# Kernel optimization log

Hardware: AMD Instinct MI355X
Metric: run time of the kernel (lower is better)

The kernel has to match this reference:

```python
import jax, jax.numpy as jnp
import numpy as np


def _conv_valid(x, w):
    # x: [B, Cin, H, W], w: [Cout, Cin, K, K], stride 1, no padding
    return jax.lax.conv_general_dilated(
        x, w, window_strides=(1, 1), padding='VALID',
        dimension_numbers=('NCHW', 'OIHW', 'NCHW'))


def _buggy_maxpool(x, k=2):
    # Faithful to the source MaxPool: window of size kxk slides with STRIDE 1,
    # but only the first H//k x W//k positions are kept (top-left region).
    nh = x.shape[2] // k
    nw = x.shape[3] // k
    m = jax.lax.reduce_window(
        x, -jnp.inf, jax.lax.max,
        window_dimensions=(1, 1, k, k),
        window_strides=(1, 1, 1, 1),
        padding='VALID')  # [B, C, H-k+1, W-k+1]
    return m[:, :, :nh, :nw]


def setup_inputs() -> dict:
    key = jax.random.key(0)
    ks = jax.random.split(key, 9)
    B = 8192
    x = jax.random.normal(ks[0], (B, 3, 32, 32), dtype=jnp.float32)
    s = 0.1
    conv1_w = jax.random.normal(ks[1], (6, 3, 5, 5), dtype=jnp.float32) * s
    conv2_w = jax.random.normal(ks[2], (16, 6, 5, 5), dtype=jnp.float32) * s
    fc1_w = jax.random.normal(ks[3], (120, 400), dtype=jnp.float32) * s
    fc1_b = jax.random.normal(ks[4], (120,), dtype=jnp.float32) * s
    fc2_w = jax.random.normal(ks[5], (84, 120), dtype=jnp.float32) * s
    fc2_b = jax.random.normal(ks[6], (84,), dtype=jnp.float32) * s
    fc3_w = jax.random.normal(ks[7], (10, 84), dtype=jnp.float32) * s
    fc3_b = jax.random.normal(ks[8], (10,), dtype=jnp.float32) * s
    return {
        'x': x,
        'conv1_w': conv1_w, 'conv2_w': conv2_w,
        'fc1_w': fc1_w, 'fc1_b': fc1_b,
        'fc2_w': fc2_w, 'fc2_b': fc2_b,
        'fc3_w': fc3_w, 'fc3_b': fc3_b,
    }


def reference(x, conv1_w, conv2_w, fc1_w, fc1_b, fc2_w, fc2_b, fc3_w, fc3_b):
    h = _buggy_maxpool(jax.nn.relu(_conv_valid(x, conv1_w)))   # [B,6,14,14]
    h = _buggy_maxpool(jax.nn.relu(_conv_valid(h, conv2_w)))   # [B,16,5,5]
    h = h.reshape(-1, 16 * 5 * 5)                              # [B,400]
    h = jax.nn.relu(h @ fc1_w.T + fc1_b)                       # [B,120]
    h = jax.nn.relu(h @ fc2_w.T + fc2_b)                       # [B,84]
    return h @ fc3_w.T + fc3_b                                 # [B,10]
```

## Files before the change

kernel.cpp:

```cpp
#include <hip/hip_runtime.h>


typedef float v2f __attribute__((ext_vector_type(2)));
__device__ __forceinline__ v2f mk2(float a, float b) { v2f t; t.x = a; t.y = b; return t; }
__device__ __forceinline__ v2f shfl2(v2f v, int src) {
    v2f r; r.x = __shfl(v.x, src, 64); r.y = __shfl(v.y, src, 64); return r;
}

constexpr int THREADS = 256;
constexpr int IPB = 4;

constexpr int W1P_OFF = 0;
constexpr int W2P_OFF = 452;
constexpr int IMG_BASE = 2852;
constexpr int XS_OFF = 0;
constexpr int P1_OFF = 0;
constexpr int P2_OFF = 900;
constexpr int F1_OFF = 0;
constexpr int F2_OFF = 128;
constexpr int IMG_STRIDE = 1300;
constexpr int LDS_FLOATS = IMG_BASE + IPB * IMG_STRIDE;

__device__ __forceinline__ void wave_sync() {
    asm volatile("s_waitcnt lgkmcnt(0)" ::: "memory");
}

extern "C" __global__ __launch_bounds__(THREADS, 4)
void lenet_fused(const float* __restrict__ x,
                 const float* __restrict__ w1,
                 const float* __restrict__ w2,
                 const float* __restrict__ fc1w, const float* __restrict__ fc1b,
                 const float* __restrict__ fc2w, const float* __restrict__ fc2b,
                 const float* __restrict__ fc3w, const float* __restrict__ fc3b,
                 float* __restrict__ out)
{
    __shared__ __align__(16) float lds[LDS_FLOATS];
    const int tid  = threadIdx.x;
    const int lane = tid & 63;
    const int wv   = tid >> 6;
    const int img0 = blockIdx.x * IPB;
    const v2f zero2 = mk2(0.f, 0.f);

    for (int i = tid; i < 450; i += THREADS) {
        int ocp = i / 150, rem = i - ocp * 150, k = rem >> 1, h = rem & 1;
        lds[W1P_OFF + i] = w1[(2 * ocp + h) * 75 + k];
    }
    for (int i = tid; i < 2400; i += THREADS) {
        int ocp = i / 300, rem = i - ocp * 300, k = rem >> 1, h = rem & 1;
        lds[W2P_OFF + i] = w2[(2 * ocp + h) * 150 + k];
    }

    float* base = lds + IMG_BASE + wv * IMG_STRIDE;
    {
        const float4* xg = (const float4*)(x + (size_t)(img0 + wv) * 3072);
        float4* xs4 = (float4*)(base + XS_OFF);
        for (int i = lane; i < 225; i += 64) {
            int c = i / 75, rem = i - c * 75;
            int r = rem / 5, c4 = rem - r * 5;
            xs4[i] = xg[c * 256 + r * 8 + c4];
        }
    }
    __syncthreads();

    float* p1 = base + P1_OFF;

    {
        const int l   = (lane < 33) ? lane : 32;
        const int ocp = l / 11;
        const int r   = l - ocp * 11;
        const float4* xs4 = (const float4*)(base + XS_OFF);
        const v2f* w1p = (const v2f*)(lds + W1P_OFF);

        v2f acc[11];
        #pragma unroll
        for (int c = 0; c < 11; ++c) acc[c] = zero2;

        float4 Xa = xs4[r * 5 + 0], Xb = xs4[r * 5 + 1],
               Xc = xs4[r * 5 + 2], Xd = xs4[r * 5 + 3];
        v2f W0[5];
        #pragma unroll
        for (int kc = 0; kc < 5; ++kc) W0[kc] = w1p[ocp * 75 + kc];

        #pragma unroll
        for (int i = 0; i < 15; ++i) {
            float4 Na, Nb, Nc, Nd; v2f W1r[5];
            if (i < 14) {
                const int ci = (i + 1) / 5, kr = (i + 1) % 5;
                const int b = ci * 75 + (r + kr) * 5;
                Na = xs4[b]; Nb = xs4[b + 1]; Nc = xs4[b + 2]; Nd = xs4[b + 3];
                #pragma unroll
                for (int kc = 0; kc < 5; ++kc)
                    W1r[kc] = w1p[ocp * 75 + (i + 1) * 5 + kc];
            }
            float xv[16];
            xv[0]=Xa.x; xv[1]=Xa.y; xv[2]=Xa.z;  xv[3]=Xa.w;
            xv[4]=Xb.x; xv[5]=Xb.y; xv[6]=Xb.z;  xv[7]=Xb.w;
            xv[8]=Xc.x; xv[9]=Xc.y; xv[10]=Xc.z; xv[11]=Xc.w;
            xv[12]=Xd.x; xv[13]=Xd.y; xv[14]=Xd.z; xv[15]=Xd.w;
            #pragma unroll
            for (int kc = 0; kc < 5; ++kc)
                #pragma unroll
                for (int c = 0; c < 11; ++c)
                    acc[c] = __builtin_elementwise_fma(
                        mk2(xv[c + kc], xv[c + kc]), W0[kc], acc[c]);
            if (i < 14) {
                Xa = Na; Xb = Nb; Xc = Nc; Xd = Nd;
                #pragma unroll
                for (int kc = 0; kc < 5; ++kc) W0[kc] = W1r[kc];
            }
        }

        v2f a[11], pm[10], m[10];
        #pragma unroll
        for (int c = 0; c < 11; ++c) a[c] = __builtin_elementwise_max(acc[c], zero2);
        #pragma unroll
        for (int c = 0; c < 10; ++c) pm[c] = __builtin_elementwise_max(a[c], a[c + 1]);
        #pragma unroll
        for (int c = 0; c < 10; ++c)
            m[c] = __builtin_elementwise_max(pm[c], shfl2(pm[c], lane + 1));
        wave_sync();
        if (r < 10) {
            const int oc0 = ocp * 2;
            float2* d0 = (float2*)(p1 + oc0 * 120 + r * 12);
            float2* d1 = (float2*)(p1 + (oc0 + 1) * 120 + r * 12);
            #pragma unroll
            for (int j = 0; j < 5; ++j) {
                d0[j] = make_float2(m[2 * j].x, m[2 * j + 1].x);
                d1[j] = make_float2(m[2 * j].y, m[2 * j + 1].y);
            }
        }
    }
    wave_sync();

    float* p2 = base + P2_OFF;
    {
        const int l   = (lane < 48) ? lane : 47;
        const int ocp = l / 6;
        const int r   = l - ocp * 6;
        const float4* p14 = (const float4*)p1;
        const float2* p12 = (const float2*)p1;
        const v2f* w2p = (const v2f*)(lds + W2P_OFF);

        v2f acc[6];
        #pragma unroll
        for (int c = 0; c < 6; ++c) acc[c] = zero2;

        float4 Xa = p14[r * 3 + 0], Xb = p14[r * 3 + 1];
        float2 Xc = p12[r * 6 + 4];
        v2f W0[5];
        #pragma unroll
        for (int kc = 0; kc < 5; ++kc) W0[kc] = w2p[ocp * 150 + kc];

        #pragma unroll
        for (int i = 0; i < 30; ++i) {
            float4 Na, Nb; float2 Nc; v2f W1r[5];
            if (i < 29) {
                const int ci = (i + 1) / 5, kr = (i + 1) % 5;
                Na = p14[ci * 30 + (r + kr) * 3 + 0];
                Nb = p14[ci * 30 + (r + kr) * 3 + 1];
                Nc = p12[ci * 60 + (r + kr) * 6 + 4];
                #pragma unroll
                for (int kc = 0; kc < 5; ++kc)
                    W1r[kc] = w2p[ocp * 150 + (i + 1) * 5 + kc];
            }
            float xv[10];
            xv[0]=Xa.x; xv[1]=Xa.y; xv[2]=Xa.z; xv[3]=Xa.w;
            xv[4]=Xb.x; xv[5]=Xb.y; xv[6]=Xb.z; xv[7]=Xb.w;
            xv[8]=Xc.x; xv[9]=Xc.y;
            #pragma unroll
            for (int kc = 0; kc < 5; ++kc)
                #pragma unroll
                for (int c = 0; c < 6; ++c)
                    acc[c] = __builtin_elementwise_fma(
                        mk2(xv[c + kc], xv[c + kc]), W0[kc], acc[c]);
            if (i < 29) {
                Xa = Na; Xb = Nb; Xc = Nc;
                #pragma unroll
                for (int kc = 0; kc < 5; ++kc) W0[kc] = W1r[kc];
            }
        }

        v2f a[6], pm[5], m[5];
        #pragma unroll
        for (int c = 0; c < 6; ++c) a[c] = __builtin_elementwise_max(acc[c], zero2);
        #pragma unroll
        for (int c = 0; c < 5; ++c) pm[c] = __builtin_elementwise_max(a[c], a[c + 1]);
        #pragma unroll
        for (int c = 0; c < 5; ++c)
            m[c] = __builtin_elementwise_max(pm[c], shfl2(pm[c], lane + 1));
        if (r < 5) {
            const int oc0 = ocp * 2;
            #pragma unroll
            for (int c = 0; c < 5; ++c) {
                p2[oc0 * 25 + r * 5 + c]       = m[c].x;
                p2[(oc0 + 1) * 25 + r * 5 + c] = m[c].y;
            }
        }
    }
    __syncthreads();

    float* scr = lds + W2P_OFF;
    if (tid < 240) {
        const int row  = tid >> 1;
        const int half = tid & 1;
        const float4* wrow = (const float4*)(fc1w + row * 400) + half * 50;
        const float4* a0p = (const float4*)(lds + IMG_BASE + 0 * IMG_STRIDE + P2_OFF) + half * 50;
        const float4* a1p = (const float4*)(lds + IMG_BASE + 1 * IMG_STRIDE + P2_OFF) + half * 50;
        const float4* a2p = (const float4*)(lds + IMG_BASE + 2 * IMG_STRIDE + P2_OFF) + half * 50;
        const float4* a3p = (const float4*)(lds + IMG_BASE + 3 * IMG_STRIDE + P2_OFF) + half * 50;
        v2f acc0 = zero2, acc1 = zero2, acc2 = zero2, acc3 = zero2;
        #pragma unroll 4
        for (int k = 0; k < 50; ++k) {
            float4 w4 = wrow[k];
            const v2f wxy = mk2(w4.x, w4.y), wzw = mk2(w4.z, w4.w);
            float4 a0 = a0p[k], a1 = a1p[k], a2 = a2p[k], a3 = a3p[k];
            acc0 = __builtin_elementwise_fma(mk2(a0.x, a0.y), wxy, acc0);
            acc0 = __builtin_elementwise_fma(mk2(a0.z, a0.w), wzw, acc0);
            acc1 = __builtin_elementwise_fma(mk2(a1.x, a1.y), wxy, acc1);
            acc1 = __builtin_elementwise_fma(mk2(a1.z, a1.w), wzw, acc1);
            acc2 = __builtin_elementwise_fma(mk2(a2.x, a2.y), wxy, acc2);
            acc2 = __builtin_elementwise_fma(mk2(a2.z, a2.w), wzw, acc2);
            acc3 = __builtin_elementwise_fma(mk2(a3.x, a3.y), wxy, acc3);
            acc3 = __builtin_elementwise_fma(mk2(a3.z, a3.w), wzw, acc3);
        }
        scr[0 * 240 + row * 2 + half] = acc0.x + acc0.y;
        scr[1 * 240 + row * 2 + half] = acc1.x + acc1.y;
        scr[2 * 240 + row * 2 + half] = acc2.x + acc2.y;
        scr[3 * 240 + row * 2 + half] = acc3.x + acc3.y;
    }
    __syncthreads();

    if (tid < 120) {
        const float b = fc1b[tid];
        #pragma unroll
        for (int im = 0; im < 4; ++im) {
            float v = scr[im * 240 + tid * 2] + scr[im * 240 + tid * 2 + 1] + b;
            lds[IMG_BASE + im * IMG_STRIDE + F1_OFF + tid] = fmaxf(v, 0.f);
        }
    }
    __syncthreads();

    if (tid < 84) {
        const int row = tid;
        const float4* wrow = (const float4*)(fc2w + row * 120);
        const float bz = fc2b[row];
        v2f acc0 = zero2, acc1 = zero2, acc2 = zero2, acc3 = zero2;
        const float4* f0 = (const float4*)(lds + IMG_BASE + 0 * IMG_STRIDE + F1_OFF);
        const float4* f1 = (const float4*)(lds + IMG_BASE + 1 * IMG_STRIDE + F1_OFF);
        const float4* f2 = (const float4*)(lds + IMG_BASE + 2 * IMG_STRIDE + F1_OFF);
        const float4* f3 = (const float4*)(lds + IMG_BASE + 3 * IMG_STRIDE + F1_OFF);
        #pragma unroll 2
        for (int k = 0; k < 30; ++k) {
            float4 w4 = wrow[k];
            const v2f wxy = mk2(w4.x, w4.y), wzw = mk2(w4.z, w4.w);
            float4 a0 = f0[k], a1 = f1[k], a2 = f2[k], a3 = f3[k];
            acc0 = __builtin_elementwise_fma(mk2(a0.x, a0.y), wxy, acc0);
            acc0 = __builtin_elementwise_fma(mk2(a0.z, a0.w), wzw, acc0);
            acc1 = __builtin_elementwise_fma(mk2(a1.x, a1.y), wxy, acc1);
            acc1 = __builtin_elementwise_fma(mk2(a1.z, a1.w), wzw, acc1);
            acc2 = __builtin_elementwise_fma(mk2(a2.x, a2.y), wxy, acc2);
            acc2 = __builtin_elementwise_fma(mk2(a2.z, a2.w), wzw, acc2);
            acc3 = __builtin_elementwise_fma(mk2(a3.x, a3.y), wxy, acc3);
            acc3 = __builtin_elementwise_fma(mk2(a3.z, a3.w), wzw, acc3);
        }
        lds[IMG_BASE + 0 * IMG_STRIDE + F2_OFF + row] = fmaxf(acc0.x + acc0.y + bz, 0.f);
        lds[IMG_BASE + 1 * IMG_STRIDE + F2_OFF + row] = fmaxf(acc1.x + acc1.y + bz, 0.f);
        lds[IMG_BASE + 2 * IMG_STRIDE + F2_OFF + row] = fmaxf(acc2.x + acc2.y + bz, 0.f);
        lds[IMG_BASE + 3 * IMG_STRIDE + F2_OFF + row] = fmaxf(acc3.x + acc3.y + bz, 0.f);
    }
    __syncthreads();

    if (tid < 40) {
        const int im  = tid / 10;
        const int row = tid - im * 10;
        const float4* wrow = (const float4*)(fc3w + row * 84);
        const float4* f2 = (const float4*)(lds + IMG_BASE + im * IMG_STRIDE + F2_OFF);
        v2f acc = zero2;
        #pragma unroll
        for (int k = 0; k < 21; ++k) {
            float4 w4 = wrow[k];
            float4 a = f2[k];
            acc = __builtin_elementwise_fma(mk2(a.x, a.y), mk2(w4.x, w4.y), acc);
            acc = __builtin_elementwise_fma(mk2(a.z, a.w), mk2(w4.z, w4.w), acc);
        }
        out[(size_t)(img0 + im) * 10 + row] = acc.x + acc.y + fc3b[row];
    }
}

extern "C" void kernel_launch(void* const* d_in, const int* in_sizes, int n_in,
                              void* d_out, int out_size, void* d_ws, size_t ws_size,
                              hipStream_t stream) {
    const float* x    = (const float*)d_in[0];
    const float* w1   = (const float*)d_in[1];
    const float* w2   = (const float*)d_in[2];
    const float* fc1w = (const float*)d_in[3];
    const float* fc1b = (const float*)d_in[4];
    const float* fc2w = (const float*)d_in[5];
    const float* fc2b = (const float*)d_in[6];
    const float* fc3w = (const float*)d_in[7];
    const float* fc3b = (const float*)d_in[8];
    float* out = (float*)d_out;

    const int B = in_sizes[0] / 3072;
    const int grid = B / IPB;
    lenet_fused<<<grid, THREADS, 0, stream>>>(x, w1, w2, fc1w, fc1b,
                                              fc2w, fc2b, fc3w, fc3b, out);
}
```

Measured before the change: 234.7 us.

## Process two images per wave to reuse conv weights and amortize FC loads

Raises images per block from 4 to 8, so each wave computes conv1 and conv2 for two images and shares the same weight registers across both. The FC layers now accumulate eight images per loaded weight row, halving the global weight traffic per image. The LDS layout is tightened (smaller image stride, fc1 scratch moved to offset 0) and launch bounds drop to 2 blocks per SM. The conv loops also lose the software prefetch of the next row and weights. Costs are higher register pressure, fewer resident blocks, and more serialized work per wave.

```diff
diff --git a/kernel.cpp b/kernel.cpp
--- a/kernel.cpp
+++ b/kernel.cpp
@@ -8,24 +8,24 @@
 }
 
 constexpr int THREADS = 256;
-constexpr int IPB = 4;
+constexpr int IPB = 8;
 
 constexpr int W1P_OFF = 0;
 constexpr int W2P_OFF = 452;
 constexpr int IMG_BASE = 2852;
 constexpr int XS_OFF = 0;
 constexpr int P1_OFF = 0;
-constexpr int P2_OFF = 900;
+constexpr int P2_OFF = 720;
 constexpr int F1_OFF = 0;
 constexpr int F2_OFF = 128;
-constexpr int IMG_STRIDE = 1300;
+constexpr int IMG_STRIDE = 1120;
 constexpr int LDS_FLOATS = IMG_BASE + IPB * IMG_STRIDE;
 
 __device__ __forceinline__ void wave_sync() {
     asm volatile("s_waitcnt lgkmcnt(0)" ::: "memory");
 }
 
-extern "C" __global__ __launch_bounds__(THREADS, 4)
+extern "C" __global__ __launch_bounds__(THREADS, 2)
 void lenet_fused(const float* __restrict__ x,
                  const float* __restrict__ w1,
                  const float* __restrict__ w2,
@@ -50,190 +50,206 @@
         lds[W2P_OFF + i] = w2[(2 * ocp + h) * 150 + k];
     }
 
-    float* base = lds + IMG_BASE + wv * IMG_STRIDE;
+    float* baseA = lds + IMG_BASE + (wv * 2) * IMG_STRIDE;
+    float* baseB = baseA + IMG_STRIDE;
     {
-        const float4* xg = (const float4*)(x + (size_t)(img0 + wv) * 3072);
-        float4* xs4 = (float4*)(base + XS_OFF);
+        const float4* xgA = (const float4*)(x + (size_t)(img0 + wv * 2) * 3072);
+        const float4* xgB = (const float4*)(x + (size_t)(img0 + wv * 2 + 1) * 3072);
+        float4* dA = (float4*)(baseA + XS_OFF);
+        float4* dB = (float4*)(baseB + XS_OFF);
         for (int i = lane; i < 225; i += 64) {
             int c = i / 75, rem = i - c * 75;
             int r = rem / 5, c4 = rem - r * 5;
-            xs4[i] = xg[c * 256 + r * 8 + c4];
-        }
-    }
-    __syncthreads();
-
-    float* p1 = base + P1_OFF;
+            int src = c * 256 + r * 8 + c4;
+            dA[i] = xgA[src];
+            dB[i] = xgB[src];
+        }
+    }
+    __syncthreads();
+
+    float* p1A = baseA + P1_OFF;
+    float* p1B = baseB + P1_OFF;
 
     {
         const int l   = (lane < 33) ? lane : 32;
         const int ocp = l / 11;
         const int r   = l - ocp * 11;
-        const float4* xs4 = (const float4*)(base + XS_OFF);
+        const float4* xsA = (const float4*)(baseA + XS_OFF);
+        const float4* xsB = (const float4*)(baseB + XS_OFF);
         const v2f* w1p = (const v2f*)(lds + W1P_OFF);
 
-        v2f acc[11];
-        #pragma unroll
-        for (int c = 0; c < 11; ++c) acc[c] = zero2;
-
-        float4 Xa = xs4[r * 5 + 0], Xb = xs4[r * 5 + 1],
-               Xc = xs4[r * 5 + 2], Xd = xs4[r * 5 + 3];
-        v2f W0[5];
-        #pragma unroll
-        for (int kc = 0; kc < 5; ++kc) W0[kc] = w1p[ocp * 75 + kc];
+        v2f accA[11], accB[11];
+        #pragma unroll
+        for (int c = 0; c < 11; ++c) { accA[c] = zero2; accB[c] = zero2; }
 
         #pragma unroll
         for (int i = 0; i < 15; ++i) {
-            float4 Na, Nb, Nc, Nd; v2f W1r[5];
-            if (i < 14) {
-                const int ci = (i + 1) / 5, kr = (i + 1) % 5;
-                const int b = ci * 75 + (r + kr) * 5;
-                Na = xs4[b]; Nb = xs4[b + 1]; Nc = xs4[b + 2]; Nd = xs4[b + 3];
+            const int ci = i / 5, kr = i - ci * 5;
+            const int b = ci * 75 + (r + kr) * 5;
+            float4 A0 = xsA[b], A1 = xsA[b + 1], A2 = xsA[b + 2], A3 = xsA[b + 3];
+            float4 B0 = xsB[b], B1 = xsB[b + 1], B2 = xsB[b + 2], B3 = xsB[b + 3];
+            v2f W[5];
+            #pragma unroll
+            for (int kc = 0; kc < 5; ++kc) W[kc] = w1p[ocp * 75 + i * 5 + kc];
+            float xa[16], xb[16];
+            xa[0]=A0.x; xa[1]=A0.y; xa[2]=A0.z;  xa[3]=A0.w;
+            xa[4]=A1.x; xa[5]=A1.y; xa[6]=A1.z;  xa[7]=A1.w;
+            xa[8]=A2.x; xa[9]=A2.y; xa[10]=A2.z; xa[11]=A2.w;
+            xa[12]=A3.x; xa[13]=A3.y; xa[14]=A3.z; xa[15]=A3.w;
+            xb[0]=B0.x; xb[1]=B0.y; xb[2]=B0.z;  xb[3]=B0.w;
+            xb[4]=B1.x; xb[5]=B1.y; xb[6]=B1.z;  xb[7]=B1.w;
+            xb[8]=B2.x; xb[9]=B2.y; xb[10]=B2.z; xb[11]=B2.w;
+            xb[12]=B3.x; xb[13]=B3.y; xb[14]=B3.z; xb[15]=B3.w;
+            #pragma unroll
+            for (int kc = 0; kc < 5; ++kc) {
                 #pragma unroll
-                for (int kc = 0; kc < 5; ++kc)
-                    W1r[kc] = w1p[ocp * 75 + (i + 1) * 5 + kc];
-            }
-            float xv[16];
-            xv[0]=Xa.x; xv[1]=Xa.y; xv[2]=Xa.z;  xv[3]=Xa.w;
-            xv[4]=Xb.x; xv[5]=Xb.y; xv[6]=Xb.z;  xv[7]=Xb.w;
-            xv[8]=Xc.x; xv[9]=Xc.y; xv[10]=Xc.z; xv[11]=Xc.w;
-            xv[12]=Xd.x; xv[13]=Xd.y; xv[14]=Xd.z; xv[15]=Xd.w;
-            #pragma unroll
-            for (int kc = 0; kc < 5; ++kc)
-                #pragma unroll
-                for (int c = 0; c < 11; ++c)
-                    acc[c] = __builtin_elementwise_fma(
-                        mk2(xv[c + kc], xv[c + kc]), W0[kc], acc[c]);
-            if (i < 14) {
-                Xa = Na; Xb = Nb; Xc = Nc; Xd = Nd;
-                #pragma unroll
-                for (int kc = 0; kc < 5; ++kc) W0[kc] = W1r[kc];
-            }
-        }
-
-        v2f a[11], pm[10], m[10];
-        #pragma unroll
-        for (int c = 0; c < 11; ++c) a[c] = __builtin_elementwise_max(acc[c], zero2);
-        #pragma unroll
-        for (int c = 0; c < 10; ++c) pm[c] = __builtin_elementwise_max(a[c], a[c + 1]);
-        #pragma unroll
-        for (int c = 0; c < 10; ++c)
-            m[c] = __builtin_elementwise_max(pm[c], shfl2(pm[c], lane + 1));
+                for (int c = 0; c < 11; ++c) {
+                    accA[c] = __builtin_elementwise_fma(
+                        mk2(xa[c + kc], xa[c + kc]), W[kc], accA[c]);
+                    accB[c] = __builtin_elementwise_fma(
+                        mk2(xb[c + kc], xb[c + kc]), W[kc], accB[c]);
+                }
+            }
+        }
+
+        v2f pmA[10], pmB[10], mA[10], mB[10];
+        #pragma unroll
+        for (int c = 0; c < 10; ++c) {
+            v2f aA0 = __builtin_elementwise_max(accA[c], zero2);
+            v2f aA1 = __builtin_elementwise_max(accA[c + 1], zero2);
+            pmA[c] = __builtin_elementwise_max(aA0, aA1);
+            v2f aB0 = __builtin_elementwise_max(accB[c], zero2);
+            v2f aB1 = __builtin_elementwise_max(accB[c + 1], zero2);
+            pmB[c] = __builtin_elementwise_max(aB0, aB1);
+        }
+        #pragma unroll
+        for (int c = 0; c < 10; ++c) {
+            mA[c] = __builtin_elementwise_max(pmA[c], shfl2(pmA[c], lane + 1));
+            mB[c] = __builtin_elementwise_max(pmB[c], shfl2(pmB[c], lane + 1));
+        }
         wave_sync();
         if (r < 10) {
             const int oc0 = ocp * 2;
-            float2* d0 = (float2*)(p1 + oc0 * 120 + r * 12);
-            float2* d1 = (float2*)(p1 + (oc0 + 1) * 120 + r * 12);
+            float2* dA0 = (float2*)(p1A + oc0 * 120 + r * 12);
+            float2* dA1 = (float2*)(p1A + (oc0 + 1) * 120 + r * 12);
+            float2* dB0 = (float2*)(p1B + oc0 * 120 + r * 12);
+            float2* dB1 = (float2*)(p1B + (oc0 + 1) * 120 + r * 12);
             #pragma unroll
             for (int j = 0; j < 5; ++j) {
-                d0[j] = make_float2(m[2 * j].x, m[2 * j + 1].x);
-                d1[j] = make_float2(m[2 * j].y, m[2 * j + 1].y);
+                dA0[j] = make_float2(mA[2 * j].x, mA[2 * j + 1].x);
+                dA1[j] = make_float2(mA[2 * j].y, mA[2 * j + 1].y);
+                dB0[j] = make_float2(mB[2 * j].x, mB[2 * j + 1].x);
+                dB1[j] = make_float2(mB[2 * j].y, mB[2 * j + 1].y);
             }
         }
     }
     wave_sync();
 
-    float* p2 = base + P2_OFF;
+    float* p2A = baseA + P2_OFF;
+    float* p2B = baseB + P2_OFF;
     {
         const int l   = (lane < 48) ? lane : 47;
         const int ocp = l / 6;
         const int r   = l - ocp * 6;
-        const float4* p14 = (const float4*)p1;
-        const float2* p12 = (const float2*)p1;
+        const float4* pA4 = (const float4*)p1A;
+        const float2* pA2 = (const float2*)p1A;
+        const float4* pB4 = (const float4*)p1B;
+        const float2* pB2 = (const float2*)p1B;
         const v2f* w2p = (const v2f*)(lds + W2P_OFF);
 
-        v2f acc[6];
-        #pragma unroll
-        for (int c = 0; c < 6; ++c) acc[c] = zero2;
-
-        float4 Xa = p14[r * 3 + 0], Xb = p14[r * 3 + 1];
-        float2 Xc = p12[r * 6 + 4];
-        v2f W0[5];
-        #pragma unroll
-        for (int kc = 0; kc < 5; ++kc) W0[kc] = w2p[ocp * 150 + kc];
+        v2f accA[6], accB[6];
+        #pragma unroll
+        for (int c = 0; c < 6; ++c) { accA[c] = zero2; accB[c] = zero2; }
 
         #pragma unroll
         for (int i = 0; i < 30; ++i) {
-            float4 Na, Nb; float2 Nc; v2f W1r[5];
-            if (i < 29) {
-                const int ci = (i + 1) / 5, kr = (i + 1) % 5;
-                Na = p14[ci * 30 + (r + kr) * 3 + 0];
-                Nb = p14[ci * 30 + (r + kr) * 3 + 1];
-                Nc = p12[ci * 60 + (r + kr) * 6 + 4];
+            const int ci = i / 5, kr = i - ci * 5;
+            float4 A0 = pA4[ci * 30 + (r + kr) * 3 + 0];
+            float4 A1 = pA4[ci * 30 + (r + kr) * 3 + 1];
+            float2 A2 = pA2[ci * 60 + (r + kr) * 6 + 4];
+            float4 B0 = pB4[ci * 30 + (r + kr) * 3 + 0];
+            float4 B1 = pB4[ci * 30 + (r + kr) * 3 + 1];
+            float2 B2 = pB2[ci * 60 + (r + kr) * 6 + 4];
+            v2f W[5];
+            #pragma unroll
+            for (int kc = 0; kc < 5; ++kc) W[kc] = w2p[ocp * 150 + i * 5 + kc];
+            float xa[10], xb[10];
+            xa[0]=A0.x; xa[1]=A0.y; xa[2]=A0.z; xa[3]=A0.w;
+            xa[4]=A1.x; xa[5]=A1.y; xa[6]=A1.z; xa[7]=A1.w;
+            xa[8]=A2.x; xa[9]=A2.y;
+            xb[0]=B0.x; xb[1]=B0.y; xb[2]=B0.z; xb[3]=B0.w;
+            xb[4]=B1.x; xb[5]=B1.y; xb[6]=B1.z; xb[7]=B1.w;
+            xb[8]=B2.x; xb[9]=B2.y;
+            #pragma unroll
+            for (int kc = 0; kc < 5; ++kc) {
                 #pragma unroll
-                for (int kc = 0; kc < 5; ++kc)
-                    W1r[kc] = w2p[ocp * 150 + (i + 1) * 5 + kc];
-            }
-            float xv[10];
-            xv[0]=Xa.x; xv[1]=Xa.y; xv[2]=Xa.z; xv[3]=Xa.w;
-            xv[4]=Xb.x; xv[5]=Xb.y; xv[6]=Xb.z; xv[7]=Xb.w;
-            xv[8]=Xc.x; xv[9]=Xc.y;
-            #pragma unroll
-            for (int kc = 0; kc < 5; ++kc)
-                #pragma unroll
-                for (int c = 0; c < 6; ++c)
-                    acc[c] = __builtin_elementwise_fma(
-                        mk2(xv[c + kc], xv[c + kc]), W0[kc], acc[c]);
-            if (i < 29) {
-                Xa = Na; Xb = Nb; Xc = Nc;
-                #pragma unroll
-                for (int kc = 0; kc < 5; ++kc) W0[kc] = W1r[kc];
-            }
-        }
-
-        v2f a[6], pm[5], m[5];
-        #pragma unroll
-        for (int c = 0; c < 6; ++c) a[c] = __builtin_elementwise_max(acc[c], zero2);
-        #pragma unroll
-        for (int c = 0; c < 5; ++c) pm[c] = __builtin_elementwise_max(a[c], a[c + 1]);
-        #pragma unroll
-        for (int c = 0; c < 5; ++c)
-            m[c] = __builtin_elementwise_max(pm[c], shfl2(pm[c], lane + 1));
+                for (int c = 0; c < 6; ++c) {
+                    accA[c] = __builtin_elementwise_fma(
+                        mk2(xa[c + kc], xa[c + kc]), W[kc], accA[c]);
+                    accB[c] = __builtin_elementwise_fma(
+                        mk2(xb[c + kc], xb[c + kc]), W[kc], accB[c]);
+                }
+            }
+        }
+
+        v2f pmA[5], pmB[5], mA[5], mB[5];
+        #pragma unroll
+        for (int c = 0; c < 5; ++c) {
+            v2f aA0 = __builtin_elementwise_max(accA[c], zero2);
+            v2f aA1 = __builtin_elementwise_max(accA[c + 1], zero2);
+            pmA[c] = __builtin_elementwise_max(aA0, aA1);
+            v2f aB0 = __builtin_elementwise_max(accB[c], zero2);
+            v2f aB1 = __builtin_elementwise_max(accB[c + 1], zero2);
+            pmB[c] = __builtin_elementwise_max(aB0, aB1);
+        }
+        #pragma unroll
+        for (int c = 0; c < 5; ++c) {
+            mA[c] = __builtin_elementwise_max(pmA[c], shfl2(pmA[c], lane + 1));
+            mB[c] = __builtin_elementwise_max(pmB[c], shfl2(pmB[c], lane + 1));
+        }
         if (r < 5) {
             const int oc0 = ocp * 2;
             #pragma unroll
             for (int c = 0; c < 5; ++c) {
-                p2[oc0 * 25 + r * 5 + c]       = m[c].x;
-                p2[(oc0 + 1) * 25 + r * 5 + c] = m[c].y;
-            }
-        }
-    }
-    __syncthreads();
-
-    float* scr = lds + W2P_OFF;
+                p2A[oc0 * 25 + r * 5 + c]       = mA[c].x;
+                p2A[(oc0 + 1) * 25 + r * 5 + c] = mA[c].y;
+                p2B[oc0 * 25 + r * 5 + c]       = mB[c].x;
+                p2B[(oc0 + 1) * 25 + r * 5 + c] = mB[c].y;
+            }
+        }
+    }
+    __syncthreads();
+
+    float* scr = lds;
     if (tid < 240) {
         const int row  = tid >> 1;
         const int half = tid & 1;
         const float4* wrow = (const float4*)(fc1w + row * 400) + half * 50;
-        const float4* a0p = (const float4*)(lds + IMG_BASE + 0 * IMG_STRIDE + P2_OFF) + half * 50;
-        const float4* a1p = (const float4*)(lds + IMG_BASE + 1 * IMG_STRIDE + P2_OFF) + half * 50;
-        const float4* a2p = (const float4*)(lds + IMG_BASE + 2 * IMG_STRIDE + P2_OFF) + half * 50;
-        const float4* a3p = (const float4*)(lds + IMG_BASE + 3 * IMG_STRIDE + P2_OFF) + half * 50;
-        v2f acc0 = zero2, acc1 = zero2, acc2 = zero2, acc3 = zero2;
-        #pragma unroll 4
+        v2f acc[8];
+        #pragma unroll
+        for (int im = 0; im < 8; ++im) acc[im] = zero2;
+        #pragma unroll 2
         for (int k = 0; k < 50; ++k) {
             float4 w4 = wrow[k];
             const v2f wxy = mk2(w4.x, w4.y), wzw = mk2(w4.z, w4.w);
-            float4 a0 = a0p[k], a1 = a1p[k], a2 = a2p[k], a3 = a3p[k];
-            acc0 = __builtin_elementwise_fma(mk2(a0.x, a0.y), wxy, acc0);
-            acc0 = __builtin_elementwise_fma(mk2(a0.z, a0.w), wzw, acc0);
-            acc1 = __builtin_elementwise_fma(mk2(a1.x, a1.y), wxy, acc1);
-            acc1 = __builtin_elementwise_fma(mk2(a1.z, a1.w), wzw, acc1);
-            acc2 = __builtin_elementwise_fma(mk2(a2.x, a2.y), wxy, acc2);
-            acc2 = __builtin_elementwise_fma(mk2(a2.z, a2.w), wzw, acc2);
-            acc3 = __builtin_elementwise_fma(mk2(a3.x, a3.y), wxy, acc3);
-            acc3 = __builtin_elementwise_fma(mk2(a3.z, a3.w), wzw, acc3);
-        }
-        scr[0 * 240 + row * 2 + half] = acc0.x + acc0.y;
-        scr[1 * 240 + row * 2 + half] = acc1.x + acc1.y;
-        scr[2 * 240 + row * 2 + half] = acc2.x + acc2.y;
-        scr[3 * 240 + row * 2 + half] = acc3.x + acc3.y;
+            #pragma unroll
+            for (int im = 0; im < 8; ++im) {
+                const float4* ap = (const float4*)(lds + IMG_BASE + im * IMG_STRIDE + P2_OFF) + half * 50;
+                float4 a = ap[k];
+                acc[im] = __builtin_elementwise_fma(mk2(a.x, a.y), wxy, acc[im]);
+                acc[im] = __builtin_elementwise_fma(mk2(a.z, a.w), wzw, acc[im]);
+            }
+        }
+        #pragma unroll
+        for (int im = 0; im < 8; ++im)
+            scr[im * 240 + row * 2 + half] = acc[im].x + acc[im].y;
     }
     __syncthreads();
 
     if (tid < 120) {
         const float b = fc1b[tid];
         #pragma unroll
-        for (int im = 0; im < 4; ++im) {
+        for (int im = 0; im < 8; ++im) {
             float v = scr[im * 240 + tid * 2] + scr[im * 240 + tid * 2 + 1] + b;
             lds[IMG_BASE + im * IMG_STRIDE + F1_OFF + tid] = fmaxf(v, 0.f);
         }
@@ -244,33 +260,29 @@
         const int row = tid;
         const float4* wrow = (const float4*)(fc2w + row * 120);
         const float bz = fc2b[row];
-        v2f acc0 = zero2, acc1 = zero2, acc2 = zero2, acc3 = zero2;
-        const float4* f0 = (const float4*)(lds + IMG_BASE + 0 * IMG_STRIDE + F1_OFF);
-        const float4* f1 = (const float4*)(lds + IMG_BASE + 1 * IMG_STRIDE + F1_OFF);
-        const float4* f2 = (const float4*)(lds + IMG_BASE + 2 * IMG_STRIDE + F1_OFF);
-        const float4* f3 = (const float4*)(lds + IMG_BASE + 3 * IMG_STRIDE + F1_OFF);
+        v2f acc[8];
+        #pragma unroll
+        for (int im = 0; im < 8; ++im) acc[im] = zero2;
         #pragma unroll 2
         for (int k = 0; k < 30; ++k) {
             float4 w4 = wrow[k];
             const v2f wxy = mk2(w4.x, w4.y), wzw = mk2(w4.z, w4.w);
-            float4 a0 = f0[k], a1 = f1[k], a2 = f2[k], a3 = f3[k];
-            acc0 = __builtin_elementwise_fma(mk2(a0.x, a0.y), wxy, acc0);
-            acc0 = __builtin_elementwise_fma(mk2(a0.z, a0.w), wzw, acc0);
-            acc1 = __builtin_elementwise_fma(mk2(a1.x, a1.y), wxy, acc1);
-            acc1 = __builtin_elementwise_fma(mk2(a1.z, a1.w), wzw, acc1);
-            acc2 = __builtin_elementwise_fma(mk2(a2.x, a2.y), wxy, acc2);
-            acc2 = __builtin_elementwise_fma(mk2(a2.z, a2.w), wzw, acc2);
-            acc3 = __builtin_elementwise_fma(mk2(a3.x, a3.y), wxy, acc3);
-            acc3 = __builtin_elementwise_fma(mk2(a3.z, a3.w), wzw, acc3);
-        }
-        lds[IMG_BASE + 0 * IMG_STRIDE + F2_OFF + row] = fmaxf(acc0.x + acc0.y + bz, 0.f);
-        lds[IMG_BASE + 1 * IMG_STRIDE + F2_OFF + row] = fmaxf(acc1.x + acc1.y + bz, 0.f);
-        lds[IMG_BASE + 2 * IMG_STRIDE + F2_OFF + row] = fmaxf(acc2.x + acc2.y + bz, 0.f);
-        lds[IMG_BASE + 3 * IMG_STRIDE + F2_OFF + row] = fmaxf(acc3.x + acc3.y + bz, 0.f);
-    }
-    __syncthreads();
-
-    if (tid < 40) {
+            #pragma unroll
+            for (int im = 0; im < 8; ++im) {
+                const float4* fp = (const float4*)(lds + IMG_BASE + im * IMG_STRIDE + F1_OFF);
+                float4 a = fp[k];
+                acc[im] = __builtin_elementwise_fma(mk2(a.x, a.y), wxy, acc[im]);
+                acc[im] = __builtin_elementwise_fma(mk2(a.z, a.w), wzw, acc[im]);
+            }
+        }
+        #pragma unroll
+        for (int im = 0; im < 8; ++im)
+            lds[IMG_BASE + im * IMG_STRIDE + F2_OFF + row] =
+                fmaxf(acc[im].x + acc[im].y + bz, 0.f);
+    }
+    __syncthreads();
+
+    if (tid < 80) {
         const int im  = tid / 10;
         const int row = tid - im * 10;
         const float4* wrow = (const float4*)(fc3w + row * 84);
```

Result: faster. 215.9 us (-8.0%).
